# Kernel tuning notes

Measured on AMD Instinct MI355X. Metric: run time of the kernel, lower is better.

The kernel has to match this reference:

```python
import jax, jax.numpy as jnp
import numpy as np

LAYER_SIZES = [256, 256, 256]
SPLIT_HALF = True
B, F0, D = 512, 32, 32


def setup_inputs() -> dict:
    key = jax.random.key(0)
    ks = jax.random.split(key, 7)
    field_nums = [F0]
    for i, s in enumerate(LAYER_SIZES):
        field_nums.append(s // 2 if (SPLIT_HALF and i != len(LAYER_SIZES) - 1) else (s // 2 if SPLIT_HALF else s))
    # field_nums = [32, 128, 128, 128] (last entry unused for weights)
    inp = {
        'feat': jax.random.normal(ks[0], (B, F0, D), dtype=jnp.float32),
        'W0': jax.random.normal(ks[1], (LAYER_SIZES[0], field_nums[0], F0), dtype=jnp.float32) * 0.05,
        'b0': jnp.zeros((LAYER_SIZES[0],), dtype=jnp.float32),
        'W1': jax.random.normal(ks[2], (LAYER_SIZES[1], field_nums[1], F0), dtype=jnp.float32) * 0.05,
        'b1': jnp.zeros((LAYER_SIZES[1],), dtype=jnp.float32),
        'W2': jax.random.normal(ks[3], (LAYER_SIZES[2], field_nums[2], F0), dtype=jnp.float32) * 0.05,
        'b2': jnp.zeros((LAYER_SIZES[2],), dtype=jnp.float32),
    }
    return inp


def _cin_layer(h, feat, W, b):
    # h: [B,H,D], feat: [B,F0,D], W: [K,H,F0], b: [K] -> out [B,K,D]
    # outer product per embedding dim, then 1x1 conv (full [H,F0] contraction)
    z = jnp.einsum('bid,bjd->bdij', h, feat)          # [B,D,H,F0]
    out = jnp.einsum('bdij,kij->bkd', z, W) + b[None, :, None]
    return jax.nn.relu(out)


def reference(feat, W0, b0, W1, b1, W2, b2):
    Ws = [W0, W1, W2]
    bs = [b0, b1, b2]
    h = feat
    p = []
    n_layers = len(LAYER_SIZES)
    for l, K in enumerate(LAYER_SIZES):
        out = _cin_layer(h, feat, Ws[l], bs[l])        # [B,K,D]
        if SPLIT_HALF and l != n_layers - 1:
            h = out[:, :K // 2, :]
            direct = out[:, K // 2:, :]
        else:
            direct = out
            h = out
        p.append(direct)
    return jnp.concatenate(p, axis=1).sum(-1)          # [B, sum of direct sizes]
```

## Files before the change

### kernel.cpp

```cpp
#include <hip/hip_runtime.h>
#include <hip/hip_fp16.h>
#include <stdint.h>


typedef _Float16 half8_t __attribute__((ext_vector_type(8)));
typedef float f32x4 __attribute__((ext_vector_type(4)));
typedef uint32_t u32x4 __attribute__((ext_vector_type(4)));

union H8 {
  half8_t h;
  uint32_t u[4];
  u32x4 q;
};

#define AS1 __attribute__((address_space(1)))
#define AS3 __attribute__((address_space(3)))

static __device__ __forceinline__ uint32_t pkmul(uint32_t x, uint32_t y) {
  __half2 a = __builtin_bit_cast(__half2, x);
  __half2 b = __builtin_bit_cast(__half2, y);
  __half2 r = __hmul2(a, b);
  return __builtin_bit_cast(uint32_t, r);
}

__global__ void prep_kernel(const float* __restrict__ W0, const float* __restrict__ W1,
                            const float* __restrict__ W2, const float* __restrict__ feat,
                            uint16_t* __restrict__ Wt0, uint16_t* __restrict__ Wt1,
                            uint16_t* __restrict__ Wt2,
                            uint16_t* __restrict__ F16, uint16_t* __restrict__ Fpack) {
  int blk = blockIdx.x;
  if (blk < 4608) {
    const float* W; uint16_t* Wt; int FLsh, base;
    if (blk < 512)       { W = W0; Wt = Wt0; FLsh = 5; base = 0; }
    else if (blk < 2560) { W = W1; Wt = Wt1; FLsh = 7; base = 512; }
    else                 { W = W2; Wt = Wt2; FLsh = 7; base = 2560; }
    int idx2 = (blk - base) * 256 + threadIdx.x;
    float2 xy = *(const float2*)(W + (size_t)idx2 * 2);
    int j2 = idx2 & 15;
    int i = (idx2 >> 4) & ((1 << FLsh) - 1);
    int k = idx2 >> (4 + FLsh);
    __half2 h2 = __floats2half2_rn(xy.x, xy.y);
    int g = j2 >> 2, kr = k & 15, kt = k >> 4;
    uint32_t* wt32 = (uint32_t*)Wt;
    wt32[(((size_t)i * 16 + kt) * 64 + g * 16 + kr) * 4 + (j2 & 3)] = *(uint32_t*)&h2;
  } else {
    int m = (blk - 4608) * 256 + threadIdx.x;
    int b = m >> 5, d = m & 31;
    const float* fb = feat + (size_t)b * 1024 + d;
    uint16_t hs[32];
#pragma unroll
    for (int j = 0; j < 32; ++j)
      hs[j] = __half_as_ushort(__float2half(fb[j * 32]));
    int pidx = (m >> 5) * 16 + (m & 15);
    int hf = (m >> 4) & 1;
#pragma unroll
    for (int j = 0; j < 32; ++j)
      Fpack[((size_t)j * 8192 + pidx) * 2 + hf] = hs[j];
#pragma unroll
    for (int c = 0; c < 4; ++c) {
      u32x4 q;
      q[0] = (uint32_t)hs[c * 8 + 0] | ((uint32_t)hs[c * 8 + 1] << 16);
      q[1] = (uint32_t)hs[c * 8 + 2] | ((uint32_t)hs[c * 8 + 3] << 16);
      q[2] = (uint32_t)hs[c * 8 + 4] | ((uint32_t)hs[c * 8 + 5] << 16);
      q[3] = (uint32_t)hs[c * 8 + 6] | ((uint32_t)hs[c * 8 + 7] << 16);
      *(u32x4*)(F16 + (size_t)m * 32 + c * 8) = q;
    }
  }
}

__global__ __launch_bounds__(1024) void gemm_cin(
    const uint32_t* __restrict__ hsrc,
    int hblock, int hstride,
    const uint16_t* __restrict__ wt,
    const uint16_t* __restrict__ f16m,
    const float* __restrict__ bias,
    uint32_t* __restrict__ hout,
    float* __restrict__ outp,
    int FL, int obase, int klo) {
  __shared__ __align__(16) char smem[65536];
  char* hlds = smem + 32768;
  const int tid = threadIdx.x;
  const int lane = tid & 63, w = tid >> 6;
  const int lr = lane & 15, hi = lane >> 4;
  const int bx = blockIdx.x;
  const int mt = bx >> 1, kh = bx & 1;
  const int m0 = mt * 128;
  const int FLm = FL - 1;
  const int phase = (bx * 37) & FLm;
  const int mw = w >> 2, kw = w & 3;
  const bool stager = (w < 8);

  const uint32_t* hb = hsrc + (size_t)mt * hblock;
  for (int qq = tid; qq < FL * 16; qq += 1024) {
    int i = qq >> 4, q4 = qq & 15;
    __builtin_amdgcn_global_load_lds(
        (const AS1 uint32_t*)(hb + (size_t)i * hstride + q4 * 4),
        (AS3 uint32_t*)(hlds + qq * 16), 16, 0, 0);
  }
  H8 ff0, ff1;
  ff0.q = *(const u32x4*)(f16m + ((size_t)m0 + mw * 32 + lr) * 32 + hi * 8);
  ff1.q = *(const u32x4*)(f16m + ((size_t)m0 + mw * 32 + 16 + lr) * 32 + hi * 8);

  const char* wbase = (const char*)wt + kh * 8192;
  if (stager) {
#pragma unroll
    for (int r = 0; r < 3; ++r) {
      int sl = (r + phase) & FLm;
      __builtin_amdgcn_global_load_lds(
          (const AS1 uint32_t*)(wbase + (size_t)sl * 16384 + w * 1024 + lane * 16),
          (AS3 uint32_t*)(smem + r * 8192 + w * 1024 + lane * 16), 16, 0, 0);
    }
  } else {
    asm volatile("s_waitcnt vmcnt(0)" ::: "memory");
  }

  f32x4 acc00 = {0.f, 0.f, 0.f, 0.f}, acc01 = acc00, acc10 = acc00, acc11 = acc00;

  for (int t = 0; t < FL; ++t) {
    const int sl = (t + phase) & FLm;
    if (stager) { asm volatile("s_waitcnt vmcnt(2)" ::: "memory"); }
    asm volatile("s_barrier" ::: "memory");
    const char* buf = smem + (t & 3) * 8192;
    H8 wf0, wf1;
    wf0.q = *(const u32x4*)(buf + (kw * 2 + 0) * 1024 + lane * 16);
    wf1.q = *(const u32x4*)(buf + (kw * 2 + 1) * 1024 + lane * 16);
    uint32_t hp = *(const uint32_t*)(hlds + (sl * 64 + mw * 16 + lr) * 4);
    if (stager) {
      int sl3 = (t + 3 + phase) & FLm;
      __builtin_amdgcn_global_load_lds(
          (const AS1 uint32_t*)(wbase + (size_t)sl3 * 16384 + w * 1024 + lane * 16),
          (AS3 uint32_t*)(smem + ((t + 3) & 3) * 8192 + w * 1024 + lane * 16), 16, 0, 0);
    }
    uint32_t e0 = __builtin_amdgcn_perm(hp, hp, 0x01000100u);
    uint32_t e1 = __builtin_amdgcn_perm(hp, hp, 0x03020302u);
    H8 a0, a1;
#pragma unroll
    for (int c = 0; c < 4; ++c) {
      a0.u[c] = pkmul(ff0.u[c], e0);
      a1.u[c] = pkmul(ff1.u[c], e1);
    }
    acc00 = __builtin_amdgcn_mfma_f32_16x16x32_f16(wf0.h, a0.h, acc00, 0, 0, 0);
    acc01 = __builtin_amdgcn_mfma_f32_16x16x32_f16(wf0.h, a1.h, acc01, 0, 0, 0);
    acc10 = __builtin_amdgcn_mfma_f32_16x16x32_f16(wf1.h, a0.h, acc10, 0, 0, 0);
    acc11 = __builtin_amdgcn_mfma_f32_16x16x32_f16(wf1.h, a1.h, acc11, 0, 0, 0);
  }

  float bv[2][4];
#pragma unroll
  for (int kf = 0; kf < 2; ++kf)
#pragma unroll
    for (int r = 0; r < 4; ++r)
      bv[kf][r] = bias[kh * 128 + kw * 32 + kf * 16 + hi * 4 + r];
  float v[2][2][4];
#pragma unroll
  for (int r = 0; r < 4; ++r) {
    float x;
    x = acc00[r] + bv[0][r]; v[0][0][r] = x > 0.f ? x : 0.f;
    x = acc01[r] + bv[0][r]; v[0][1][r] = x > 0.f ? x : 0.f;
    x = acc10[r] + bv[1][r]; v[1][0][r] = x > 0.f ? x : 0.f;
    x = acc11[r] + bv[1][r]; v[1][1][r] = x > 0.f ? x : 0.f;
  }

  if (hout != nullptr && kh == 0) {
#pragma unroll
    for (int kf = 0; kf < 2; ++kf)
#pragma unroll
      for (int r = 0; r < 4; ++r) {
        int k_loc = kw * 32 + kf * 16 + hi * 4 + r;
        uint32_t lo = __half_as_ushort(__float2half(v[kf][0][r]));
        uint32_t hi16 = __half_as_ushort(__float2half(v[kf][1][r]));
        hout[(size_t)mt * 8192 + k_loc * 64 + mw * 16 + lr] = lo | (hi16 << 16);
      }
  }

  int b = mt * 4 + mw;
#pragma unroll
  for (int kf = 0; kf < 2; ++kf) {
    float s[4];
#pragma unroll
    for (int r = 0; r < 4; ++r) {
      float x = v[kf][0][r] + v[kf][1][r];
      x += __shfl_xor(x, 1);
      x += __shfl_xor(x, 2);
      x += __shfl_xor(x, 4);
      x += __shfl_xor(x, 8);
      s[r] = x;
    }
    if (lr == 0) {
      int kbase = kh * 128 + kw * 32 + kf * 16 + hi * 4;
#pragma unroll
      for (int r = 0; r < 4; ++r) {
        int k = kbase + r;
        if (k >= klo) outp[(size_t)b * 512 + obase + k - klo] = s[r];
      }
    }
  }
  asm volatile("s_waitcnt vmcnt(0)" ::: "memory");
}

extern "C" void kernel_launch(void* const* d_in, const int* in_sizes, int n_in,
                              void* d_out, int out_size, void* d_ws, size_t ws_size,
                              hipStream_t stream) {
  const float* feat = (const float*)d_in[0];
  const float* W0 = (const float*)d_in[1];
  const float* b0 = (const float*)d_in[2];
  const float* W1 = (const float*)d_in[3];
  const float* b1 = (const float*)d_in[4];
  const float* W2 = (const float*)d_in[5];
  const float* b2 = (const float*)d_in[6];
  float* out = (float*)d_out;
  char* ws = (char*)d_ws;

  uint16_t* Wt0  = (uint16_t*)(ws + 0x000000);
  uint16_t* Wt1  = (uint16_t*)(ws + 0x080000);
  uint16_t* Wt2  = (uint16_t*)(ws + 0x280000);
  uint16_t* F16  = (uint16_t*)(ws + 0x480000);
  uint16_t* Fpk  = (uint16_t*)(ws + 0x580000);
  uint32_t* h1   = (uint32_t*)(ws + 0x680000);
  uint32_t* h2   = (uint32_t*)(ws + 0xA80000);

  prep_kernel<<<4672, 256, 0, stream>>>(W0, W1, W2, feat, Wt0, Wt1, Wt2, F16, Fpk);

  gemm_cin<<<256, 1024, 0, stream>>>((const uint32_t*)Fpk, 64, 8192, Wt0, F16, b0,
                                     h1, out, 32, 0, 128);
  gemm_cin<<<256, 1024, 0, stream>>>(h1, 8192, 64, Wt1, F16, b1,
                                     h2, out, 128, 128, 128);
  gemm_cin<<<256, 1024, 0, stream>>>(h2, 8192, 64, Wt2, F16, b2,
                                     (uint32_t*)nullptr, out, 128, 256, 0);
}
```

Measured before the change: 106.7 us.

## Retile CIN GEMM so each block covers all 256 outputs for 64 rows

```diff
diff --git a/kernel.cpp b/kernel.cpp
--- a/kernel.cpp
+++ b/kernel.cpp
@@ -27,7 +27,7 @@
                             const float* __restrict__ W2, const float* __restrict__ feat,
                             uint16_t* __restrict__ Wt0, uint16_t* __restrict__ Wt1,
                             uint16_t* __restrict__ Wt2,
-                            uint16_t* __restrict__ F16, uint16_t* __restrict__ Fpack) {
+                            uint16_t* __restrict__ F16, uint16_t* __restrict__ Fpk) {
   int blk = blockIdx.x;
   if (blk < 4608) {
     const float* W; uint16_t* Wt; int FLsh, base;
@@ -51,11 +51,10 @@
 #pragma unroll
     for (int j = 0; j < 32; ++j)
       hs[j] = __half_as_ushort(__float2half(fb[j * 32]));
-    int pidx = (m >> 5) * 16 + (m & 15);
-    int hf = (m >> 4) & 1;
+    int mt = m >> 6, g = (m >> 5) & 1, plr = m & 15, hf = (m >> 4) & 1;
 #pragma unroll
     for (int j = 0; j < 32; ++j)
-      Fpack[((size_t)j * 8192 + pidx) * 2 + hf] = hs[j];
+      Fpk[(((size_t)mt * 32 + j) * 32 + plr * 2 + g) * 2 + hf] = hs[j];
 #pragma unroll
     for (int c = 0; c < 4; ++c) {
       u32x4 q;
@@ -68,132 +67,118 @@
   }
 }
 
-__global__ __launch_bounds__(1024) void gemm_cin(
+__global__ __launch_bounds__(1024, 4) void gemm_cin(
     const uint32_t* __restrict__ hsrc,
-    int hblock, int hstride,
+    int hblock,
     const uint16_t* __restrict__ wt,
     const uint16_t* __restrict__ f16m,
     const float* __restrict__ bias,
     uint32_t* __restrict__ hout,
     float* __restrict__ outp,
     int FL, int obase, int klo) {
-  __shared__ __align__(16) char smem[65536];
-  char* hlds = smem + 32768;
+  __shared__ __align__(16) char smem[81920];
+  char* hlds = smem + 65536;
   const int tid = threadIdx.x;
   const int lane = tid & 63, w = tid >> 6;
   const int lr = lane & 15, hi = lane >> 4;
-  const int bx = blockIdx.x;
-  const int mt = bx >> 1, kh = bx & 1;
-  const int m0 = mt * 128;
+  const int mt = blockIdx.x;
+  const int m0 = mt * 64;
   const int FLm = FL - 1;
-  const int phase = (bx * 37) & FLm;
-  const int mw = w >> 2, kw = w & 3;
-  const bool stager = (w < 8);
+  const int phase = ((mt & 7) * (FL >> 3)) & FLm;
 
   const uint32_t* hb = hsrc + (size_t)mt * hblock;
-  for (int qq = tid; qq < FL * 16; qq += 1024) {
-    int i = qq >> 4, q4 = qq & 15;
+  for (int qq = tid; qq < FL * 8; qq += 1024)
+    __builtin_amdgcn_global_load_lds((const AS1 uint32_t*)(hb + qq * 4),
+                                     (AS3 uint32_t*)(hlds + qq * 16), 16, 0, 0);
+
+  H8 ff[4];
+#pragma unroll
+  for (int mf = 0; mf < 4; ++mf)
+    ff[mf].q = *(const u32x4*)(f16m + (size_t)(m0 + mf * 16 + lr) * 32 + hi * 8);
+
+  const char* wbase = (const char*)wt;
+#pragma unroll
+  for (int r = 0; r < 3; ++r) {
+    int sl = (r + phase) & FLm;
     __builtin_amdgcn_global_load_lds(
-        (const AS1 uint32_t*)(hb + (size_t)i * hstride + q4 * 4),
-        (AS3 uint32_t*)(hlds + qq * 16), 16, 0, 0);
-  }
-  H8 ff0, ff1;
-  ff0.q = *(const u32x4*)(f16m + ((size_t)m0 + mw * 32 + lr) * 32 + hi * 8);
-  ff1.q = *(const u32x4*)(f16m + ((size_t)m0 + mw * 32 + 16 + lr) * 32 + hi * 8);
-
-  const char* wbase = (const char*)wt + kh * 8192;
-  if (stager) {
-#pragma unroll
-    for (int r = 0; r < 3; ++r) {
-      int sl = (r + phase) & FLm;
-      __builtin_amdgcn_global_load_lds(
-          (const AS1 uint32_t*)(wbase + (size_t)sl * 16384 + w * 1024 + lane * 16),
-          (AS3 uint32_t*)(smem + r * 8192 + w * 1024 + lane * 16), 16, 0, 0);
-    }
-  } else {
-    asm volatile("s_waitcnt vmcnt(0)" ::: "memory");
-  }
-
-  f32x4 acc00 = {0.f, 0.f, 0.f, 0.f}, acc01 = acc00, acc10 = acc00, acc11 = acc00;
+        (const AS1 uint32_t*)(wbase + (size_t)sl * 16384 + tid * 16),
+        (AS3 uint32_t*)(smem + r * 16384 + tid * 16), 16, 0, 0);
+  }
+
+  f32x4 acc[4];
+#pragma unroll
+  for (int mf = 0; mf < 4; ++mf) acc[mf] = (f32x4){0.f, 0.f, 0.f, 0.f};
 
   for (int t = 0; t < FL; ++t) {
     const int sl = (t + phase) & FLm;
-    if (stager) { asm volatile("s_waitcnt vmcnt(2)" ::: "memory"); }
+    const int sl3 = (t + 3 + phase) & FLm;
+    __builtin_amdgcn_global_load_lds(
+        (const AS1 uint32_t*)(wbase + (size_t)sl3 * 16384 + tid * 16),
+        (AS3 uint32_t*)(smem + ((t + 3) & 3) * 16384 + tid * 16), 16, 0, 0);
+    asm volatile("s_waitcnt vmcnt(3)" ::: "memory");
     asm volatile("s_barrier" ::: "memory");
-    const char* buf = smem + (t & 3) * 8192;
-    H8 wf0, wf1;
-    wf0.q = *(const u32x4*)(buf + (kw * 2 + 0) * 1024 + lane * 16);
-    wf1.q = *(const u32x4*)(buf + (kw * 2 + 1) * 1024 + lane * 16);
-    uint32_t hp = *(const uint32_t*)(hlds + (sl * 64 + mw * 16 + lr) * 4);
-    if (stager) {
-      int sl3 = (t + 3 + phase) & FLm;
-      __builtin_amdgcn_global_load_lds(
-          (const AS1 uint32_t*)(wbase + (size_t)sl3 * 16384 + w * 1024 + lane * 16),
-          (AS3 uint32_t*)(smem + ((t + 3) & 3) * 8192 + w * 1024 + lane * 16), 16, 0, 0);
-    }
-    uint32_t e0 = __builtin_amdgcn_perm(hp, hp, 0x01000100u);
-    uint32_t e1 = __builtin_amdgcn_perm(hp, hp, 0x03020302u);
-    H8 a0, a1;
+
+    const char* buf = smem + (t & 3) * 16384;
+    uint2 hq = *(const uint2*)(hlds + sl * 128 + lr * 8);
+    H8 wf;
+    wf.q = *(const u32x4*)(buf + w * 1024 + lane * 16);
+    uint32_t e0 = __builtin_amdgcn_perm(hq.x, hq.x, 0x01000100u);
+    uint32_t e1 = __builtin_amdgcn_perm(hq.x, hq.x, 0x03020302u);
+    uint32_t e2 = __builtin_amdgcn_perm(hq.y, hq.y, 0x01000100u);
+    uint32_t e3 = __builtin_amdgcn_perm(hq.y, hq.y, 0x03020302u);
+    H8 a0, a1, a2, a3;
 #pragma unroll
     for (int c = 0; c < 4; ++c) {
-      a0.u[c] = pkmul(ff0.u[c], e0);
-      a1.u[c] = pkmul(ff1.u[c], e1);
-    }
-    acc00 = __builtin_amdgcn_mfma_f32_16x16x32_f16(wf0.h, a0.h, acc00, 0, 0, 0);
-    acc01 = __builtin_amdgcn_mfma_f32_16x16x32_f16(wf0.h, a1.h, acc01, 0, 0, 0);
-    acc10 = __builtin_amdgcn_mfma_f32_16x16x32_f16(wf1.h, a0.h, acc10, 0, 0, 0);
-    acc11 = __builtin_amdgcn_mfma_f32_16x16x32_f16(wf1.h, a1.h, acc11, 0, 0, 0);
-  }
-
-  float bv[2][4];
-#pragma unroll
-  for (int kf = 0; kf < 2; ++kf)
-#pragma unroll
-    for (int r = 0; r < 4; ++r)
-      bv[kf][r] = bias[kh * 128 + kw * 32 + kf * 16 + hi * 4 + r];
-  float v[2][2][4];
+      a0.u[c] = pkmul(ff[0].u[c], e0);
+      a1.u[c] = pkmul(ff[1].u[c], e1);
+      a2.u[c] = pkmul(ff[2].u[c], e2);
+      a3.u[c] = pkmul(ff[3].u[c], e3);
+    }
+    acc[0] = __builtin_amdgcn_mfma_f32_16x16x32_f16(wf.h, a0.h, acc[0], 0, 0, 0);
+    acc[1] = __builtin_amdgcn_mfma_f32_16x16x32_f16(wf.h, a1.h, acc[1], 0, 0, 0);
+    acc[2] = __builtin_amdgcn_mfma_f32_16x16x32_f16(wf.h, a2.h, acc[2], 0, 0, 0);
+    acc[3] = __builtin_amdgcn_mfma_f32_16x16x32_f16(wf.h, a3.h, acc[3], 0, 0, 0);
+  }
+
+  f32x4 bv = *(const f32x4*)(bias + w * 16 + hi * 4);
+  float v[4][4];
+#pragma unroll
+  for (int mf = 0; mf < 4; ++mf)
+#pragma unroll
+    for (int r = 0; r < 4; ++r) {
+      float x = acc[mf][r] + bv[r];
+      v[mf][r] = x > 0.f ? x : 0.f;
+    }
+
+  if (hout != nullptr && w < 8) {
+#pragma unroll
+    for (int r = 0; r < 4; ++r) {
+      int k = w * 16 + hi * 4 + r;
+#pragma unroll
+      for (int g = 0; g < 2; ++g) {
+        uint32_t lo = __half_as_ushort(__float2half(v[2 * g][r]));
+        uint32_t hi16 = __half_as_ushort(__float2half(v[2 * g + 1][r]));
+        hout[(size_t)mt * 4096 + k * 32 + lr * 2 + g] = lo | (hi16 << 16);
+      }
+    }
+  }
+
+  f32x4 s0v, s1v;
 #pragma unroll
   for (int r = 0; r < 4; ++r) {
-    float x;
-    x = acc00[r] + bv[0][r]; v[0][0][r] = x > 0.f ? x : 0.f;
-    x = acc01[r] + bv[0][r]; v[0][1][r] = x > 0.f ? x : 0.f;
-    x = acc10[r] + bv[1][r]; v[1][0][r] = x > 0.f ? x : 0.f;
-    x = acc11[r] + bv[1][r]; v[1][1][r] = x > 0.f ? x : 0.f;
-  }
-
-  if (hout != nullptr && kh == 0) {
-#pragma unroll
-    for (int kf = 0; kf < 2; ++kf)
-#pragma unroll
-      for (int r = 0; r < 4; ++r) {
-        int k_loc = kw * 32 + kf * 16 + hi * 4 + r;
-        uint32_t lo = __half_as_ushort(__float2half(v[kf][0][r]));
-        uint32_t hi16 = __half_as_ushort(__float2half(v[kf][1][r]));
-        hout[(size_t)mt * 8192 + k_loc * 64 + mw * 16 + lr] = lo | (hi16 << 16);
-      }
-  }
-
-  int b = mt * 4 + mw;
-#pragma unroll
-  for (int kf = 0; kf < 2; ++kf) {
-    float s[4];
-#pragma unroll
-    for (int r = 0; r < 4; ++r) {
-      float x = v[kf][0][r] + v[kf][1][r];
-      x += __shfl_xor(x, 1);
-      x += __shfl_xor(x, 2);
-      x += __shfl_xor(x, 4);
-      x += __shfl_xor(x, 8);
-      s[r] = x;
-    }
-    if (lr == 0) {
-      int kbase = kh * 128 + kw * 32 + kf * 16 + hi * 4;
-#pragma unroll
-      for (int r = 0; r < 4; ++r) {
-        int k = kbase + r;
-        if (k >= klo) outp[(size_t)b * 512 + obase + k - klo] = s[r];
-      }
-    }
+    float x0 = v[0][r] + v[1][r];
+    x0 += __shfl_xor(x0, 1); x0 += __shfl_xor(x0, 2);
+    x0 += __shfl_xor(x0, 4); x0 += __shfl_xor(x0, 8);
+    s0v[r] = x0;
+    float x1 = v[2][r] + v[3][r];
+    x1 += __shfl_xor(x1, 1); x1 += __shfl_xor(x1, 2);
+    x1 += __shfl_xor(x1, 4); x1 += __shfl_xor(x1, 8);
+    s1v[r] = x1;
+  }
+  int k0 = w * 16 + hi * 4;
+  if (lr == 0 && k0 >= klo) {
+    *(f32x4*)(outp + (size_t)(mt * 2) * 512 + obase + k0 - klo) = s0v;
+    *(f32x4*)(outp + (size_t)(mt * 2 + 1) * 512 + obase + k0 - klo) = s1v;
   }
   asm volatile("s_waitcnt vmcnt(0)" ::: "memory");
 }
@@ -211,20 +196,20 @@
   float* out = (float*)d_out;
   char* ws = (char*)d_ws;
 
-  uint16_t* Wt0  = (uint16_t*)(ws + 0x000000);
-  uint16_t* Wt1  = (uint16_t*)(ws + 0x080000);
-  uint16_t* Wt2  = (uint16_t*)(ws + 0x280000);
-  uint16_t* F16  = (uint16_t*)(ws + 0x480000);
-  uint16_t* Fpk  = (uint16_t*)(ws + 0x580000);
-  uint32_t* h1   = (uint32_t*)(ws + 0x680000);
-  uint32_t* h2   = (uint32_t*)(ws + 0xA80000);
+  uint16_t* Wt0 = (uint16_t*)(ws + 0x000000);
+  uint16_t* Wt1 = (uint16_t*)(ws + 0x080000);
+  uint16_t* Wt2 = (uint16_t*)(ws + 0x280000);
+  uint16_t* F16 = (uint16_t*)(ws + 0x480000);
+  uint16_t* Fpk = (uint16_t*)(ws + 0x580000);
+  uint32_t* h1  = (uint32_t*)(ws + 0x680000);
+  uint32_t* h2  = (uint32_t*)(ws + 0xA80000);
 
   prep_kernel<<<4672, 256, 0, stream>>>(W0, W1, W2, feat, Wt0, Wt1, Wt2, F16, Fpk);
 
-  gemm_cin<<<256, 1024, 0, stream>>>((const uint32_t*)Fpk, 64, 8192, Wt0, F16, b0,
+  gemm_cin<<<256, 1024, 0, stream>>>((const uint32_t*)Fpk, 1024, Wt0, F16, b0,
                                      h1, out, 32, 0, 128);
-  gemm_cin<<<256, 1024, 0, stream>>>(h1, 8192, 64, Wt1, F16, b1,
+  gemm_cin<<<256, 1024, 0, stream>>>(h1, 4096, Wt1, F16, b1,
                                      h2, out, 128, 128, 128);
-  gemm_cin<<<256, 1024, 0, stream>>>(h2, 8192, 64, Wt2, F16, b2,
+  gemm_cin<<<256, 1024, 0, stream>>>(h2, 4096, Wt2, F16, b2,
                                      (uint32_t*)nullptr, out, 128, 256, 0);
 }
```

Result: slower. 142.4 us (+33.5%).
